# Kernel tuning notes

Hardware: AMD Instinct MI355X
Metric: run time of the kernel (lower is better)

The kernel has to match this reference:

```python
import jax, jax.numpy as jnp
import numpy as np

NUM_HEADS = 12

def setup_inputs() -> dict:
    key = jax.random.key(0)
    k1, k2, k3 = jax.random.split(key, 3)
    B, N, D = 16, 1024, 768
    x = jax.random.normal(k1, (B, N, D), dtype=jnp.float32)
    w_qkv = jax.random.normal(k2, (D, 3 * D), dtype=jnp.float32) * (D ** -0.5)
    b_qkv = jnp.zeros((3 * D,), dtype=jnp.float32)
    w_proj = jax.random.normal(k3, (D, D), dtype=jnp.float32) * (D ** -0.5)
    b_proj = jnp.zeros((D,), dtype=jnp.float32)
    return {"x": x, "w_qkv": w_qkv, "b_qkv": b_qkv, "w_proj": w_proj, "b_proj": b_proj}

def reference(x, w_qkv, b_qkv, w_proj, b_proj):
    B, N, D = x.shape
    H = NUM_HEADS
    Hd = D // H
    scale = Hd ** -0.5
    qkv = x @ w_qkv + b_qkv                       # (B, N, 3D)
    qkv = qkv.reshape(B, N, 3, H, Hd)
    q, k, v = qkv[:, :, 0], qkv[:, :, 1], qkv[:, :, 2]  # (B, N, H, Hd)
    attn = jnp.einsum('bnhd,bmhd->bhnm', q, k) * scale  # (B, H, N, N)
    attn = jax.nn.softmax(attn, axis=-1)
    out = jnp.einsum('bhnm,bmhd->bnhd', attn, v).reshape(B, N, D)
    return out @ w_proj + b_proj
```

## Files before the change

### kernel.cpp

```cpp
#include <hip/hip_runtime.h>


typedef _Float16 half8 __attribute__((ext_vector_type(8)));
typedef _Float16 half4 __attribute__((ext_vector_type(4)));
typedef __fp16   fp16x2 __attribute__((ext_vector_type(2)));
typedef float    f32x4  __attribute__((ext_vector_type(4)));
typedef float    f32x16 __attribute__((ext_vector_type(16)));
typedef unsigned int u32x4 __attribute__((ext_vector_type(4)));

#define DI __device__ __forceinline__

constexpr int   BATCH  = 16;
constexpr int   SEQ    = 1024;
constexpr int   DM     = 768;
constexpr int   NH     = 12;
constexpr int   HD     = 64;
constexpr float SCALE  = 0.125f;
constexpr float LOG2E  = 1.4426950408889634f;

DI void copy16(_Float16* dst, const _Float16* src) {
  *(u32x4*)dst = *(const u32x4*)src;
}

DI int pack_rtz(float a, float b) {
  union { fp16x2 h; int i; } u;
  u.h = __builtin_amdgcn_cvt_pkrtz(a, b);
  return u.i;
}

DI void gld16(const _Float16* g, _Float16* l) {
  __builtin_amdgcn_global_load_lds(
      (const __attribute__((address_space(1))) void*)g,
      (__attribute__((address_space(3))) void*)l, 16, 0, 0);
}

__global__ void cvt_wt2_kernel(const float* __restrict__ wq,
                               _Float16* __restrict__ wqT,
                               const float* __restrict__ wp,
                               _Float16* __restrict__ wpT) {
  __shared__ float tile[32][33];
  const int by = blockIdx.y;
  const float* w; _Float16* wt; int N, nb;
  if (by < 72) { w = wq; wt = wqT; N = 2304; nb = by * 32; }
  else         { w = wp; wt = wpT; N = 768;  nb = (by - 72) * 32; }
  const int K = 768;
  int kb = blockIdx.x * 32;
  int tx = threadIdx.x & 31, ty = threadIdx.x >> 5;
#pragma unroll
  for (int i = 0; i < 32; i += 8)
    tile[ty + i][tx] = w[(size_t)(kb + ty + i) * N + nb + tx];
  __syncthreads();
#pragma unroll
  for (int i = 0; i < 32; i += 8)
    wt[(size_t)(nb + ty + i) * K + kb + tx] = (_Float16)tile[tx][ty + i];
}

__launch_bounds__(256, 4)
__global__ void gemm_qkv_kernel(const float* __restrict__ X,
                                const _Float16* __restrict__ Bt,
                                const float* __restrict__ bias,
                                _Float16* __restrict__ Qo,
                                _Float16* __restrict__ Ko,
                                _Float16* __restrict__ VTo) {
  __shared__ _Float16 sh[16384];
  _Float16* Cs = sh;
  const int tid  = threadIdx.x;
  const int lin  = blockIdx.x;
  const int xcd  = lin & 7, j = lin >> 3;
  const int ct   = j % 18;
  const int m0   = ((j / 18) * 8 + xcd) * 128;
  const int n0   = ct * 128;
  const int w    = tid >> 6, lane = tid & 63;
  const int quad = lane >> 4, l15 = lane & 15;
  const int wr   = w >> 1, wc = w & 1;

  f32x4 acc[4][4] = {};

  const int g0 = tid + w * 64;
  const int r0 = g0 >> 2, s0 = g0 & 3;
  const float*    gaA = X  + (size_t)(m0 + r0) * 768 + s0 * 8;
  const _Float16* gbB = Bt + (size_t)(n0 + r0) * 768 + s0 * 8;
  const int so   = r0 * 32 + s0 * 8;
  const int ldst = w * 1024;

  auto CVT_WRITE = [&](float4 a0, float4 a1, float4 a2, float4 a3,
                       _Float16* As) {
    half8 h0, h1;
    h0[0] = (_Float16)a0.x; h0[1] = (_Float16)a0.y;
    h0[2] = (_Float16)a0.z; h0[3] = (_Float16)a0.w;
    h0[4] = (_Float16)a1.x; h0[5] = (_Float16)a1.y;
    h0[6] = (_Float16)a1.z; h0[7] = (_Float16)a1.w;
    h1[0] = (_Float16)a2.x; h1[1] = (_Float16)a2.y;
    h1[2] = (_Float16)a2.z; h1[3] = (_Float16)a2.w;
    h1[4] = (_Float16)a3.x; h1[5] = (_Float16)a3.y;
    h1[6] = (_Float16)a3.z; h1[7] = (_Float16)a3.w;
    *(half8*)(As + so)       = h0;
    *(half8*)(As + so + 512) = h1;
  };

  {
    float4 a0 = *(const float4*)(gaA);
    float4 a1 = *(const float4*)(gaA + 4);
    float4 a2 = *(const float4*)(gaA + 16 * 768);
    float4 a3 = *(const float4*)(gaA + 16 * 768 + 4);
    CVT_WRITE(a0, a1, a2, a3, sh);
    gld16(gbB,            sh + 4096 + ldst);
    gld16(gbB + 16 * 768, sh + 4096 + ldst + 512);
  }

  for (int kt = 0; kt < 24; ++kt) {
    __syncthreads();
    float4 a0, a1, a2, a3;
    if (kt < 23) {
      const int k0 = (kt + 1) * 32;
      a0 = *(const float4*)(gaA + k0);
      a1 = *(const float4*)(gaA + k0 + 4);
      a2 = *(const float4*)(gaA + k0 + 16 * 768);
      a3 = *(const float4*)(gaA + k0 + 16 * 768 + 4);
      _Float16* Bsn = sh + ((kt + 1) & 1) * 8192 + 4096;
      gld16(gbB + k0,            Bsn + ldst);
      gld16(gbB + k0 + 16 * 768, Bsn + ldst + 512);
    }

    const _Float16* As = sh + (kt & 1) * 8192;
    const _Float16* Bs = As + 4096;

    half8 af[4], bf[4];
#pragma unroll
    for (int mi = 0; mi < 4; mi++)
      af[mi] = *(const half8*)&As[(wr * 64 + mi * 16 + l15) * 32 + quad * 8];
#pragma unroll
    for (int ni = 0; ni < 4; ni++)
      bf[ni] = *(const half8*)&Bs[(wc * 64 + ni * 16 + l15) * 32 + quad * 8];
#pragma unroll
    for (int mi = 0; mi < 4; mi++)
#pragma unroll
      for (int ni = 0; ni < 4; ni++)
        acc[mi][ni] = __builtin_amdgcn_mfma_f32_16x16x32_f16(
            af[mi], bf[ni], acc[mi][ni], 0, 0, 0);

    if (kt < 23)
      CVT_WRITE(a0, a1, a2, a3, sh + ((kt + 1) & 1) * 8192);
  }
  __syncthreads();

  const float oscale = (ct < 6) ? SCALE : 1.0f;
  float bcol[4];
#pragma unroll
  for (int ni = 0; ni < 4; ni++)
    bcol[ni] = bias[n0 + wc * 64 + ni * 16 + l15];

  const int b     = m0 >> 10;
  const int nrow0 = m0 & 1023;
  const int sec   = ct / 6;
  const int h0    = (ct % 6) * 2;

#pragma unroll
  for (int p = 0; p < 2; ++p) {
    if (p) __syncthreads();
    if (wr == p) {
#pragma unroll
      for (int mi = 0; mi < 4; mi++)
#pragma unroll
        for (int ni = 0; ni < 4; ni++) {
          int col = wc * 64 + ni * 16 + l15;
          int row = mi * 16 + quad * 4;
#pragma unroll
          for (int r = 0; r < 4; r++)
            Cs[(row + r) * 136 + col] =
                (_Float16)((acc[mi][ni][r] + bcol[ni]) * oscale);
        }
    }
    __syncthreads();

    if (sec < 2) {
      _Float16* dst = (sec == 0) ? Qo : Ko;
      int row = tid >> 2, seg = tid & 3;
      int hl = seg >> 1, off32 = (seg & 1) * 32;
      _Float16* g = dst +
          ((size_t)((b * NH + h0 + hl) * SEQ + nrow0 + p * 64 + row)) * HD + off32;
      const _Float16* s = &Cs[row * 136 + hl * 64 + off32];
      copy16(g, s);
      copy16(g + 8, s + 8);
      copy16(g + 16, s + 16);
      copy16(g + 24, s + 24);
    } else {
      int c = tid & 127, half = tid >> 7;
      int hl = c >> 6, d = c & 63;
      _Float16 tmp[32];
#pragma unroll
      for (int jj = 0; jj < 32; jj++) tmp[jj] = Cs[(half * 32 + jj) * 136 + c];
      _Float16* g = VTo + ((size_t)((b * NH + h0 + hl) * HD + d)) * SEQ
                        + nrow0 + p * 64 + half * 32;
#pragma unroll
      for (int jj = 0; jj < 4; jj++)
        copy16(g + jj * 8, (const _Float16*)&tmp[jj * 8]);
    }
  }
}

__launch_bounds__(256, 2)
__global__ void attn_kernel(const _Float16* __restrict__ Q,
                            const _Float16* __restrict__ K,
                            const _Float16* __restrict__ VT,
                            _Float16* __restrict__ Oh) {
  __shared__ _Float16 smem[2][2][64 * 72];
  _Float16* OLds = &smem[0][0][0];

  const int tid = threadIdx.x;
  const int i   = blockIdx.x;
  const int bh  = (i & 7) * 24 + ((i >> 3) >> 2);
  const int q0  = ((i >> 3) & 3) * 256;
  const int b   = bh / NH, hh = bh - b * NH;
  const int w   = tid >> 6, lane = tid & 63;
  const int l31 = lane & 31, h = lane >> 5;

  const _Float16* Qg = Q  + (size_t)bh * SEQ * HD;
  const _Float16* Kg = K  + (size_t)bh * SEQ * HD;
  const _Float16* Vg = VT + (size_t)bh * HD * SEQ;

  half8 qb[2][4];
#pragma unroll
  for (int N = 0; N < 2; N++) {
    const _Float16* qrow = Qg + (size_t)(q0 + w * 64 + N * 32 + l31) * HD + h * 8;
#pragma unroll
    for (int s = 0; s < 4; s++)
      qb[N][s] = *(const half8*)(qrow + s * 16);
  }

  const int  sr  = (tid & 127) >> 1;
  const int  sp  = tid & 1;
  const bool isK = tid < 128;
  const _Float16* sg = isK ? (Kg + sr * HD + sp * 32)
                           : (Vg + (size_t)sr * SEQ + sp * 32);
  const int sstep = isK ? 64 * HD : 64;
  const int soff  = (isK ? 0 : 64 * 72) + sr * 72 + sp * 32;

  u32x4 pf[4];
#pragma unroll
  for (int c = 0; c < 4; c++) pf[c] = *(const u32x4*)(sg + c * 8);
#pragma unroll
  for (int c = 0; c < 4; c++) *(u32x4*)(&smem[0][0][0] + soff + c * 8) = pf[c];

  f32x16 of[2][2];
#pragma unroll
  for (int D = 0; D < 2; D++)
#pragma unroll
    for (int N = 0; N < 2; N++)
#pragma unroll
      for (int r = 0; r < 16; r++) of[D][N][r] = 0.f;
  float m_[2] = {-1e30f, -1e30f}, l_[2] = {0.f, 0.f};

  for (int kt = 0; kt < 16; ++kt) {
    if (kt < 15) {
      const _Float16* nsg = sg + (kt + 1) * sstep;
#pragma unroll
      for (int c = 0; c < 4; c++) pf[c] = *(const u32x4*)(nsg + c * 8);
    }
    __syncthreads();
    const _Float16* Ks = &smem[kt & 1][0][0];
    const _Float16* Vs = &smem[kt & 1][1][0];

    f32x16 sf[2][2];
#pragma unroll
    for (int M = 0; M < 2; M++)
#pragma unroll
      for (int N = 0; N < 2; N++)
#pragma unroll
        for (int r = 0; r < 16; r++) sf[M][N][r] = 0.f;
#pragma unroll
    for (int s = 0; s < 4; s++) {
      half8 ka0 = *(const half8*)&Ks[l31 * 72 + s * 16 + h * 8];
      half8 ka1 = *(const half8*)&Ks[(32 + l31) * 72 + s * 16 + h * 8];
#pragma unroll
      for (int N = 0; N < 2; N++) {
        sf[0][N] = __builtin_amdgcn_mfma_f32_32x32x16_f16(ka0, qb[N][s], sf[0][N], 0, 0, 0);
        sf[1][N] = __builtin_amdgcn_mfma_f32_32x32x16_f16(ka1, qb[N][s], sf[1][N], 0, 0, 0);
      }
    }

    float alpha[2], c1[2], tsum[2];
#pragma unroll
    for (int N = 0; N < 2; N++) {
      float tmax = -1e30f;
#pragma unroll
      for (int r = 0; r < 16; r++)
        tmax = fmaxf(tmax, fmaxf(sf[0][N][r], sf[1][N][r]));
      tmax = fmaxf(tmax, __shfl_xor(tmax, 32, 64));
      float mnew = fmaxf(m_[N], tmax);
      alpha[N] = __builtin_amdgcn_exp2f((m_[N] - mnew) * LOG2E);
      m_[N] = mnew;
      c1[N] = mnew * LOG2E;
      tsum[N] = 0.f;
    }

    int pdw[2][2][8];
#pragma unroll
    for (int M = 0; M < 2; M++)
#pragma unroll
      for (int N = 0; N < 2; N++) {
#pragma unroll
        for (int r = 0; r < 16; r++) {
          float p = __builtin_amdgcn_exp2f(sf[M][N][r] * LOG2E - c1[N]);
          sf[M][N][r] = p;
          tsum[N] += p;
        }
#pragma unroll
        for (int u = 0; u < 8; u++)
          pdw[M][N][u] = pack_rtz(sf[M][N][2 * u], sf[M][N][2 * u + 1]);
      }
#pragma unroll
    for (int N = 0; N < 2; N++) {
      tsum[N] += __shfl_xor(tsum[N], 32, 64);
      l_[N] = l_[N] * alpha[N] + tsum[N];
    }
#pragma unroll
    for (int D = 0; D < 2; D++)
#pragma unroll
      for (int N = 0; N < 2; N++)
#pragma unroll
        for (int r = 0; r < 16; r++) of[D][N][r] *= alpha[N];

#pragma unroll
    for (int t = 0; t < 4; ++t) {
      const int M = t >> 1, s2 = (t & 1) * 4;
      half8 va0 = *(const half8*)&Vs[l31 * 72 + t * 16 + h * 8];
      half8 va1 = *(const half8*)&Vs[(32 + l31) * 72 + t * 16 + h * 8];
#pragma unroll
      for (int N = 0; N < 2; N++) {
        int a0 = pdw[M][N][s2 + 0], a1 = pdw[M][N][s2 + 1];
        int a2 = pdw[M][N][s2 + 2], a3 = pdw[M][N][s2 + 3];
        int e0 = h ? a0 : a2, e1 = h ? a1 : a3;
        int r0 = __shfl_xor(e0, 32, 64), r1 = __shfl_xor(e1, 32, 64);
        union { u32x4 u; half8 hv; } bb;
        bb.u[0] = h ? r0 : a0; bb.u[1] = h ? r1 : a1;
        bb.u[2] = h ? a2 : r0; bb.u[3] = h ? a3 : r1;
        of[0][N] = __builtin_amdgcn_mfma_f32_32x32x16_f16(va0, bb.hv, of[0][N], 0, 0, 0);
        of[1][N] = __builtin_amdgcn_mfma_f32_32x32x16_f16(va1, bb.hv, of[1][N], 0, 0, 0);
      }
    }

    if (kt < 15) {
      _Float16* dst = &smem[(kt + 1) & 1][0][0] + soff;
#pragma unroll
      for (int c = 0; c < 4; c++) *(u32x4*)(dst + c * 8) = pf[c];
    }
  }

  __syncthreads();
  float inv[2] = {1.0f / l_[0], 1.0f / l_[1]};
  int* OW = (int*)OLds;
#pragma unroll
  for (int N = 0; N < 2; N++) {
    const int q_local = w * 64 + N * 32 + l31;
#pragma unroll
    for (int D = 0; D < 2; D++)
#pragma unroll
      for (int u = 0; u < 8; u++) {
        int v = pack_rtz(of[D][N][2 * u] * inv[N], of[D][N][2 * u + 1] * inv[N]);
        int dwi = 16 * D + 4 * (u >> 1) + (u & 1) + 2 * h;
        OW[q_local * 36 + dwi] = v;
      }
  }
  __syncthreads();
#pragma unroll
  for (int p = 0; p < 8; p++) {
    int q = p * 32 + (tid >> 3), c = tid & 7;
    *(u32x4*)(Oh + (size_t)(b * SEQ + q0 + q) * DM + hh * HD + c * 8) =
        *(const u32x4*)&OLds[q * 72 + c * 8];
  }
}

__launch_bounds__(256, 4)
__global__ void gemm_proj_kernel(const _Float16* __restrict__ A,
                                 const _Float16* __restrict__ Bt,
                                 const float* __restrict__ bias,
                                 float* __restrict__ out) {
  __shared__ _Float16 sh[16384];
  const int tid  = threadIdx.x;
  const int lin  = blockIdx.x;
  const int xcd  = lin & 7, j = lin >> 3;
  const int ct   = j % 6;
  const int m0   = ((j / 6) * 8 + xcd) * 128;
  const int n0   = ct * 128;
  const int w    = tid >> 6, lane = tid & 63;
  const int quad = lane >> 4, l15 = lane & 15;
  const int wr   = w >> 1, wc = w & 1;

  f32x4 acc[4][4] = {};

  const int g0 = tid + w * 64;
  const int r0 = g0 >> 2, s0 = g0 & 3;
  const _Float16* gaA = A  + (size_t)(m0 + r0) * 768 + s0 * 8;
  const _Float16* gaB = Bt + (size_t)(n0 + r0) * 768 + s0 * 8;
  const int ldst = w * 1024;

  auto STAGE = [&](int buf, int kt) {
    _Float16* As = sh + buf * 8192;
    _Float16* Bs = As + 4096;
    const _Float16* a = gaA + kt * 32;
    const _Float16* b = gaB + kt * 32;
    gld16(a,            As + ldst);
    gld16(a + 16 * 768, As + ldst + 512);
    gld16(b,            Bs + ldst);
    gld16(b + 16 * 768, Bs + ldst + 512);
  };

  STAGE(0, 0);

  for (int kt = 0; kt < 24; ++kt) {
    __syncthreads();
    if (kt < 23) STAGE((kt + 1) & 1, kt + 1);

    const _Float16* As = sh + (kt & 1) * 8192;
    const _Float16* Bs = As + 4096;

    half8 af[4], bf[4];
#pragma unroll
    for (int mi = 0; mi < 4; mi++)
      af[mi] = *(const half8*)&As[(wr * 64 + mi * 16 + l15) * 32 + quad * 8];
#pragma unroll
    for (int ni = 0; ni < 4; ni++)
      bf[ni] = *(const half8*)&Bs[(wc * 64 + ni * 16 + l15) * 32 + quad * 8];
#pragma unroll
    for (int mi = 0; mi < 4; mi++)
#pragma unroll
      for (int ni = 0; ni < 4; ni++)
        acc[mi][ni] = __builtin_amdgcn_mfma_f32_16x16x32_f16(
            af[mi], bf[ni], acc[mi][ni], 0, 0, 0);
  }

  float bcol[4];
#pragma unroll
  for (int ni = 0; ni < 4; ni++)
    bcol[ni] = bias[n0 + wc * 64 + ni * 16 + l15];
#pragma unroll
  for (int mi = 0; mi < 4; mi++)
#pragma unroll
    for (int ni = 0; ni < 4; ni++) {
      int col = n0 + wc * 64 + ni * 16 + l15;
      int row = m0 + wr * 64 + mi * 16 + quad * 4;
#pragma unroll
      for (int r = 0; r < 4; r++)
        out[(size_t)(row + r) * 768 + col] = acc[mi][ni][r] + bcol[ni];
    }
}

extern "C" void kernel_launch(void* const* d_in, const int* in_sizes, int n_in,
                              void* d_out, int out_size, void* d_ws, size_t ws_size,
                              hipStream_t stream) {
  const float* x      = (const float*)d_in[0];
  const float* w_qkv  = (const float*)d_in[1];
  const float* b_qkv  = (const float*)d_in[2];
  const float* w_proj = (const float*)d_in[3];
  const float* b_proj = (const float*)d_in[4];
  float* out = (float*)d_out;

  char* ws = (char*)d_ws;
  _Float16* wqkvT  = (_Float16*)(ws);
  _Float16* wprojT = (_Float16*)(ws + 3538944);
  _Float16* Qp     = (_Float16*)(ws + 4718592);
  _Float16* Kp     = (_Float16*)(ws + 29884416);
  _Float16* VTp    = (_Float16*)(ws + 55050240);
  _Float16* Ohp    = (_Float16*)(ws + 80216064);

  cvt_wt2_kernel<<<dim3(24, 96), 256, 0, stream>>>(w_qkv, wqkvT, w_proj, wprojT);
  gemm_qkv_kernel<<<dim3(2304), 256, 0, stream>>>(x, wqkvT, b_qkv, Qp, Kp, VTp);
  attn_kernel<<<dim3(768), 256, 0, stream>>>(Qp, Kp, VTp, Ohp);
  gemm_proj_kernel<<<dim3(768), 256, 0, stream>>>(Ohp, wprojT, b_proj, out);
}
```

Baseline: 329.4 us.

## Widen GEMM tiles to 128x256 with eight waves per block

Both the QKV and the output-projection GEMMs move from 128x128 tiles with 4 waves to 128x256 tiles with 8 waves (512 threads). Each loaded A tile (including the fp32-to-fp16 conversion of X in the QKV GEMM) is now reused across twice as many output columns, which cuts global A traffic and conversion work. The epilogue index mapping is adapted to the wider tile. In exchange, more shared memory is used per block, the grids are smaller (384 blocks for the projection), and wave-level parallelism may be less balanced.

```diff
diff --git a/kernel.cpp b/kernel.cpp
--- a/kernel.cpp
+++ b/kernel.cpp
@@ -55,74 +55,65 @@
     wt[(size_t)(nb + ty + i) * K + kb + tx] = (_Float16)tile[tx][ty + i];
 }
 
-__launch_bounds__(256, 4)
+__launch_bounds__(512, 3)
 __global__ void gemm_qkv_kernel(const float* __restrict__ X,
                                 const _Float16* __restrict__ Bt,
                                 const float* __restrict__ bias,
                                 _Float16* __restrict__ Qo,
                                 _Float16* __restrict__ Ko,
                                 _Float16* __restrict__ VTo) {
-  __shared__ _Float16 sh[16384];
+  __shared__ _Float16 sh[24576];
   _Float16* Cs = sh;
   const int tid  = threadIdx.x;
   const int lin  = blockIdx.x;
   const int xcd  = lin & 7, j = lin >> 3;
-  const int ct   = j % 18;
-  const int m0   = ((j / 18) * 8 + xcd) * 128;
-  const int n0   = ct * 128;
+  const int ct   = j % 9;
+  const int m0   = ((j / 9) * 8 + xcd) * 128;
+  const int n0   = ct * 256;
   const int w    = tid >> 6, lane = tid & 63;
   const int quad = lane >> 4, l15 = lane & 15;
-  const int wr   = w >> 1, wc = w & 1;
+  const int wr   = w >> 2, wc = w & 3;
 
   f32x4 acc[4][4] = {};
 
-  const int g0 = tid + w * 64;
-  const int r0 = g0 >> 2, s0 = g0 & 3;
-  const float*    gaA = X  + (size_t)(m0 + r0) * 768 + s0 * 8;
-  const _Float16* gbB = Bt + (size_t)(n0 + r0) * 768 + s0 * 8;
-  const int so   = r0 * 32 + s0 * 8;
+  const int rA = tid >> 2, sA = tid & 3;
+  const float* gaA = X + (size_t)(m0 + rA) * 768 + sA * 8;
+  const int so = rA * 32 + sA * 8;
+
+  const _Float16* gbB = Bt + (size_t)(n0 + ((w * 128 + lane) >> 2)) * 768
+                           + (lane & 3) * 8;
   const int ldst = w * 1024;
 
-  auto CVT_WRITE = [&](float4 a0, float4 a1, float4 a2, float4 a3,
-                       _Float16* As) {
-    half8 h0, h1;
+  auto CVT_WRITE = [&](float4 a0, float4 a1, _Float16* As) {
+    half8 h0;
     h0[0] = (_Float16)a0.x; h0[1] = (_Float16)a0.y;
     h0[2] = (_Float16)a0.z; h0[3] = (_Float16)a0.w;
     h0[4] = (_Float16)a1.x; h0[5] = (_Float16)a1.y;
     h0[6] = (_Float16)a1.z; h0[7] = (_Float16)a1.w;
-    h1[0] = (_Float16)a2.x; h1[1] = (_Float16)a2.y;
-    h1[2] = (_Float16)a2.z; h1[3] = (_Float16)a2.w;
-    h1[4] = (_Float16)a3.x; h1[5] = (_Float16)a3.y;
-    h1[6] = (_Float16)a3.z; h1[7] = (_Float16)a3.w;
-    *(half8*)(As + so)       = h0;
-    *(half8*)(As + so + 512) = h1;
+    *(half8*)(As + so) = h0;
   };
 
   {
     float4 a0 = *(const float4*)(gaA);
     float4 a1 = *(const float4*)(gaA + 4);
-    float4 a2 = *(const float4*)(gaA + 16 * 768);
-    float4 a3 = *(const float4*)(gaA + 16 * 768 + 4);
-    CVT_WRITE(a0, a1, a2, a3, sh);
+    CVT_WRITE(a0, a1, sh);
     gld16(gbB,            sh + 4096 + ldst);
     gld16(gbB + 16 * 768, sh + 4096 + ldst + 512);
   }
 
   for (int kt = 0; kt < 24; ++kt) {
     __syncthreads();
-    float4 a0, a1, a2, a3;
+    float4 a0, a1;
     if (kt < 23) {
       const int k0 = (kt + 1) * 32;
       a0 = *(const float4*)(gaA + k0);
       a1 = *(const float4*)(gaA + k0 + 4);
-      a2 = *(const float4*)(gaA + k0 + 16 * 768);
-      a3 = *(const float4*)(gaA + k0 + 16 * 768 + 4);
-      _Float16* Bsn = sh + ((kt + 1) & 1) * 8192 + 4096;
+      _Float16* Bsn = sh + ((kt + 1) & 1) * 12288 + 4096;
       gld16(gbB + k0,            Bsn + ldst);
       gld16(gbB + k0 + 16 * 768, Bsn + ldst + 512);
     }
 
-    const _Float16* As = sh + (kt & 1) * 8192;
+    const _Float16* As = sh + (kt & 1) * 12288;
     const _Float16* Bs = As + 4096;
 
     half8 af[4], bf[4];
@@ -140,11 +131,13 @@
             af[mi], bf[ni], acc[mi][ni], 0, 0, 0);
 
     if (kt < 23)
-      CVT_WRITE(a0, a1, a2, a3, sh + ((kt + 1) & 1) * 8192);
+      CVT_WRITE(a0, a1, sh + ((kt + 1) & 1) * 12288);
   }
   __syncthreads();
 
-  const float oscale = (ct < 6) ? SCALE : 1.0f;
+  const int   sec    = ct / 3;
+  const int   h0     = (ct % 3) * 4;
+  const float oscale = (sec == 0) ? SCALE : 1.0f;
   float bcol[4];
 #pragma unroll
   for (int ni = 0; ni < 4; ni++)
@@ -152,8 +145,6 @@
 
   const int b     = m0 >> 10;
   const int nrow0 = m0 & 1023;
-  const int sec   = ct / 6;
-  const int h0    = (ct % 6) * 2;
 
 #pragma unroll
   for (int p = 0; p < 2; ++p) {
@@ -167,7 +158,7 @@
           int row = mi * 16 + quad * 4;
 #pragma unroll
           for (int r = 0; r < 4; r++)
-            Cs[(row + r) * 136 + col] =
+            Cs[(row + r) * 264 + col] =
                 (_Float16)((acc[mi][ni][r] + bcol[ni]) * oscale);
         }
     }
@@ -175,23 +166,23 @@
 
     if (sec < 2) {
       _Float16* dst = (sec == 0) ? Qo : Ko;
-      int row = tid >> 2, seg = tid & 3;
+      int row = tid >> 3, seg = tid & 7;
       int hl = seg >> 1, off32 = (seg & 1) * 32;
       _Float16* g = dst +
           ((size_t)((b * NH + h0 + hl) * SEQ + nrow0 + p * 64 + row)) * HD + off32;
-      const _Float16* s = &Cs[row * 136 + hl * 64 + off32];
+      const _Float16* s = &Cs[row * 264 + hl * 64 + off32];
       copy16(g, s);
       copy16(g + 8, s + 8);
       copy16(g + 16, s + 16);
       copy16(g + 24, s + 24);
     } else {
-      int c = tid & 127, half = tid >> 7;
+      int c = tid & 255, rh = tid >> 8;
       int hl = c >> 6, d = c & 63;
       _Float16 tmp[32];
 #pragma unroll
-      for (int jj = 0; jj < 32; jj++) tmp[jj] = Cs[(half * 32 + jj) * 136 + c];
+      for (int jj = 0; jj < 32; jj++) tmp[jj] = Cs[(rh * 32 + jj) * 264 + c];
       _Float16* g = VTo + ((size_t)((b * NH + h0 + hl) * HD + d)) * SEQ
-                        + nrow0 + p * 64 + half * 32;
+                        + nrow0 + p * 64 + rh * 32;
 #pragma unroll
       for (int jj = 0; jj < 4; jj++)
         copy16(g + jj * 8, (const _Float16*)&tmp[jj * 8]);
@@ -371,39 +362,39 @@
   }
 }
 
-__launch_bounds__(256, 4)
+__launch_bounds__(512, 3)
 __global__ void gemm_proj_kernel(const _Float16* __restrict__ A,
                                  const _Float16* __restrict__ Bt,
                                  const float* __restrict__ bias,
                                  float* __restrict__ out) {
-  __shared__ _Float16 sh[16384];
+  __shared__ _Float16 sh[24576];
   const int tid  = threadIdx.x;
   const int lin  = blockIdx.x;
   const int xcd  = lin & 7, j = lin >> 3;
-  const int ct   = j % 6;
-  const int m0   = ((j / 6) * 8 + xcd) * 128;
-  const int n0   = ct * 128;
+  const int ct   = j % 3;
+  const int m0   = ((j / 3) * 8 + xcd) * 128;
+  const int n0   = ct * 256;
   const int w    = tid >> 6, lane = tid & 63;
   const int quad = lane >> 4, l15 = lane & 15;
-  const int wr   = w >> 1, wc = w & 1;
+  const int wr   = w >> 2, wc = w & 3;
 
   f32x4 acc[4][4] = {};
 
-  const int g0 = tid + w * 64;
-  const int r0 = g0 >> 2, s0 = g0 & 3;
-  const _Float16* gaA = A  + (size_t)(m0 + r0) * 768 + s0 * 8;
-  const _Float16* gaB = Bt + (size_t)(n0 + r0) * 768 + s0 * 8;
-  const int ldst = w * 1024;
+  const _Float16* gaA = A + (size_t)(m0 + ((w * 64 + lane) >> 2)) * 768
+                          + (lane & 3) * 8;
+  const int ldstA = w * 512;
+  const _Float16* gbB = Bt + (size_t)(n0 + ((w * 128 + lane) >> 2)) * 768
+                           + (lane & 3) * 8;
+  const int ldstB = w * 1024;
 
   auto STAGE = [&](int buf, int kt) {
-    _Float16* As = sh + buf * 8192;
+    _Float16* As = sh + buf * 12288;
     _Float16* Bs = As + 4096;
     const _Float16* a = gaA + kt * 32;
-    const _Float16* b = gaB + kt * 32;
-    gld16(a,            As + ldst);
-    gld16(a + 16 * 768, As + ldst + 512);
-    gld16(b,            Bs + ldst);
-    gld16(b + 16 * 768, Bs + ldst + 512);
+    const _Float16* b = gbB + kt * 32;
+    gld16(a,            As + ldstA);
+    gld16(b,            Bs + ldstB);
+    gld16(b + 16 * 768, Bs + ldstB + 512);
   };
 
   STAGE(0, 0);
@@ -412,7 +403,7 @@
     __syncthreads();
     if (kt < 23) STAGE((kt + 1) & 1, kt + 1);
 
-    const _Float16* As = sh + (kt & 1) * 8192;
+    const _Float16* As = sh + (kt & 1) * 12288;
     const _Float16* Bs = As + 4096;
 
     half8 af[4], bf[4];
@@ -465,7 +456,7 @@
   _Float16* Ohp    = (_Float16*)(ws + 80216064);
 
   cvt_wt2_kernel<<<dim3(24, 96), 256, 0, stream>>>(w_qkv, wqkvT, w_proj, wprojT);
-  gemm_qkv_kernel<<<dim3(2304), 256, 0, stream>>>(x, wqkvT, b_qkv, Qp, Kp, VTp);
+  gemm_qkv_kernel<<<dim3(1152), 512, 0, stream>>>(x, wqkvT, b_qkv, Qp, Kp, VTp);
   attn_kernel<<<dim3(768), 256, 0, stream>>>(Qp, Kp, VTp, Ohp);
-  gemm_proj_kernel<<<dim3(768), 256, 0, stream>>>(Ohp, wprojT, b_proj, out);
-}
+  gemm_proj_kernel<<<dim3(384), 512, 0, stream>>>(Ohp, wprojT, b_proj, out);
+}
```

New measurement: 299.4 us, median of 2. -9.1%, faster.
